# Kernel tuning notes

Measured on AMD Instinct MI355X. Metric: run time of the kernel, lower is better.

## Reference

```python
import jax, jax.numpy as jnp
import numpy as np
from jax import lax

N, T, E = 20000, 64, 640000
H, OUT, HEADS = 128, 64, 3
NEG_SLOPE = 0.2  # GATConv default negative_slope


def setup_inputs() -> dict:
    key = jax.random.key(0)
    ks = jax.random.split(key, 10)
    s = 0.1
    return {
        "node_features": jax.random.normal(ks[0], (N, T), jnp.float32),
        "edge_index": jax.random.randint(ks[1], (2, E), 0, N, dtype=jnp.int32),
        "edge_attributes": jax.random.uniform(ks[2], (E,), jnp.float32),
        "lstm_Wih": jax.random.normal(ks[3], (4 * H, 1), jnp.float32) * s,
        "lstm_Whh": jax.random.normal(ks[4], (4 * H, H), jnp.float32) * s,
        "lstm_bih": jnp.zeros((4 * H,), jnp.float32),
        "lstm_bhh": jnp.zeros((4 * H,), jnp.float32),
        "gcn_W": jax.random.normal(ks[5], (H, H), jnp.float32) * s,
        "gcn_b": jnp.zeros((H,), jnp.float32),
        "gat_W": jax.random.normal(ks[6], (HEADS * OUT, H), jnp.float32) * s,
        "gat_att_src": jax.random.normal(ks[7], (HEADS, OUT), jnp.float32) * s,
        "gat_att_dst": jax.random.normal(ks[8], (HEADS, OUT), jnp.float32) * s,
        "gat_b": jnp.zeros((HEADS * OUT,), jnp.float32),
    }


def _lstm_last(x, Wih, Whh, bih, bhh):
    """x: [N, T, 1] -> last hidden state [N, H] (torch gate order i,f,g,o)."""
    n = x.shape[0]
    h_dim = Whh.shape[1]
    b = bih + bhh

    def step(carry, xt):
        h, c = carry
        g = xt @ Wih.T + h @ Whh.T + b  # [N, 4H]
        i, f, gg, o = jnp.split(g, 4, axis=-1)
        c = jax.nn.sigmoid(f) * c + jax.nn.sigmoid(i) * jnp.tanh(gg)
        h = jax.nn.sigmoid(o) * jnp.tanh(c)
        return (h, c), None

    init = (jnp.zeros((n, h_dim), x.dtype), jnp.zeros((n, h_dim), x.dtype))
    (h, _), _ = lax.scan(step, init, jnp.swapaxes(x, 0, 1))
    return h


def _add_self_loops(row, col, n):
    loop = jnp.arange(n, dtype=row.dtype)
    return jnp.concatenate([row, loop]), jnp.concatenate([col, loop])


def _gcn(x, row, col, edge_weight, W, b):
    """PyG GCNConv: self-loops (weight 1), symmetric normalization, W x + b."""
    n = x.shape[0]
    row, col = _add_self_loops(row, col, n)
    ew = jnp.concatenate([edge_weight, jnp.ones((n,), edge_weight.dtype)])
    x = x @ W.T  # [N, H]
    deg = jax.ops.segment_sum(ew, col, num_segments=n)
    dinv = jnp.where(deg > 0, deg ** -0.5, 0.0)
    norm = dinv[row] * ew * dinv[col]  # [E+N]
    out = jax.ops.segment_sum(x[row] * norm[:, None], col, num_segments=n)
    return out + b


def _gat(x, row, col, W, att_src, att_dst, b):
    """PyG GATConv (concat=True): self-loops, edge softmax over incoming edges."""
    n = x.shape[0]
    heads, c = att_src.shape
    xh = (x @ W.T).reshape(n, heads, c)  # [N, Hd, C]
    a_src = jnp.einsum('nhc,hc->nh', xh, att_src)  # [N, Hd]
    a_dst = jnp.einsum('nhc,hc->nh', xh, att_dst)
    row, col = _add_self_loops(row, col, n)
    alpha = jax.nn.leaky_relu(a_src[row] + a_dst[col], NEG_SLOPE)  # [E', Hd]
    amax = jax.ops.segment_max(alpha, col, num_segments=n)
    alpha = jnp.exp(alpha - amax[col])
    denom = jax.ops.segment_sum(alpha, col, num_segments=n)
    alpha = alpha / denom[col]
    out = jax.ops.segment_sum(xh[row] * alpha[:, :, None], col, num_segments=n)
    return out.reshape(n, heads * c) + b


def reference(node_features, edge_index, edge_attributes,
              lstm_Wih, lstm_Whh, lstm_bih, lstm_bhh,
              gcn_W, gcn_b, gat_W, gat_att_src, gat_att_dst, gat_b):
    x = node_features[:, :, None]  # [N, T, 1]
    x = _lstm_last(x, lstm_Wih, lstm_Whh, lstm_bih, lstm_bhh)  # [N, H]
    x = jax.nn.relu(x)
    row, col = edge_index[0], edge_index[1]
    x = _gcn(x, row, col, edge_attributes, gcn_W, gcn_b)
    x = jax.nn.relu(x)
    x = _gat(x, row, col, gat_W, gat_att_src, gat_att_dst, gat_b)  # [N, Hd*C]
    return jnp.mean(x, axis=0, keepdims=True)  # global_mean_pool, batch=None -> [1, Hd*C]
```

## Files before the change

### kernel.cpp

```cpp
#include <hip/hip_runtime.h>


#define N_NODES 20000
#define T_STEPS 64
#define N_EDGES 640000
#define HDIM    128
#define JOUT    192
#define NEG_SLOPE 0.2f
#define EDGE_CAP 128
#define NBW     16
#define NGRP    5
#define NBB     (NBW * NGRP)
#define BTHR    640
#define NBLK    250
#define GRIDX   256
#define LDS_W     131072
#define LDS_BW    4096
#define LDS_SCR   (NGRP * 4096)
#define LDS_FLG   256
#define LDS_TOTAL (LDS_W + LDS_BW + LDS_SCR + LDS_FLG)

#define L2E  1.4426950408889634f
#define K2E  2.8853900817779268f

typedef _Float16 half8 __attribute__((ext_vector_type(8)));
typedef _Float16 half4v __attribute__((ext_vector_type(4)));
typedef _Float16 half2v __attribute__((ext_vector_type(2)));
typedef float floatx4 __attribute__((ext_vector_type(4)));

__device__ __forceinline__ float lrelu(float x) { return x > 0.f ? x : NEG_SLOPE * x; }

__global__ __launch_bounds__(256) void prep_kernel(
    const float* __restrict__ Whh, _Float16* __restrict__ Wpack,
    const float* __restrict__ gcnW, _Float16* __restrict__ WpackG,
    const float* __restrict__ gatW, _Float16* __restrict__ WpackA,
    int* __restrict__ cnt, float* __restrict__ Wgt, float* __restrict__ accum)
{
  const int b = blockIdx.x;
  const int tid = threadIdx.x;
  if (b < 32) {
    int i = b * 256 + tid;
    int tile = i >> 6, lane = i & 63;
    int nt = tile >> 2, kt = tile & 3;
    int row = nt * 16 + (lane & 15);
    int c0  = kt * 32 + (lane >> 4) * 8;
    const float sc = ((row >> 7) == 2) ? K2E : L2E;
    half8 v;
    #pragma unroll
    for (int j = 0; j < 8; ++j)
      v[j] = (_Float16)(Whh[row * 128 + c0 + j] * sc);
    *(half8*)&Wpack[(size_t)i * 8] = v;
  } else if (b < 40) {
    int i = (b - 32) * 256 + tid;
    int tile = i >> 6, lane = i & 63;
    int mt = tile >> 2, kt = tile & 3;
    int row = mt * 16 + (lane & 15);
    int c0  = kt * 32 + (lane >> 4) * 8;
    half8 v;
    #pragma unroll
    for (int j = 0; j < 8; ++j) v[j] = (_Float16)gcnW[row * 128 + c0 + j];
    *(half8*)&WpackG[(size_t)i * 8] = v;
  } else if (b < 52) {
    int i = (b - 40) * 256 + tid;
    int tile = i >> 6, lane = i & 63;
    int mt = tile >> 2, kt = tile & 3;
    int row = mt * 16 + (lane & 15);
    int c0  = kt * 32 + (lane >> 4) * 8;
    half8 v;
    #pragma unroll
    for (int j = 0; j < 8; ++j) v[j] = (_Float16)gatW[row * 128 + c0 + j];
    *(half8*)&WpackA[(size_t)i * 8] = v;
  } else {
    int i = (b - 52) * 256 + tid;
    if (i < N_NODES) {
      cnt[i] = 0;
      *(float4*)&Wgt[i * 4] = make_float4(0.f, 0.f, 0.f, 0.f);
    }
    if (i < JOUT) accum[i] = 0.f;
  }
}


#define INITACC(L, acc) do {                                                  \
  _Pragma("unroll") for (int g_ = 0; g_ < 4; ++g_) {                          \
    const float4 p0_ = *(const float4*)&bwRole[g_ * 128 + (L) * 16];          \
    const float4 p1_ = *(const float4*)&bwRole[g_ * 128 + (L) * 16 + 2];      \
    acc[g_][0] = p0_.x + xv * p0_.y;                                          \
    acc[g_][1] = p0_.z + xv * p0_.w;                                          \
    acc[g_][2] = p1_.x + xv * p1_.y;                                          \
    acc[g_][3] = p1_.z + xv * p1_.w;                                          \
  }                                                                           \
} while (0)

#define LDA(buf, L, KT) do {                                                  \
  _Pragma("unroll") for (int g_ = 0; g_ < 4; ++g_)                            \
    buf[g_] = *(const half8*)&WlRole[g_ * 16384 + (L) * 2048 + (KT) * 512];   \
} while (0)

#define MFA(acc, buf, KT) do {                                                \
  _Pragma("unroll") for (int g_ = 0; g_ < 4; ++g_)                            \
    acc[g_] = __builtin_amdgcn_mfma_f32_16x16x32_f16(                         \
        buf[g_], Bf[(KT)], acc[g_], 0, 0, 0);                                 \
} while (0)

#define PHASE4(L, acc) do {                                                   \
  const int cg_ = cgb + (L);                                                  \
  half4v hpack;                                                               \
  _Pragma("unroll") for (int r_ = 0; r_ < 4; ++r_) {                          \
    const float Be = __builtin_amdgcn_exp2f(-acc[0][r_]);                     \
    const float Ae = __builtin_amdgcn_exp2f(-acc[1][r_]);                     \
    const float De = __builtin_amdgcn_exp2f(acc[2][r_]);                      \
    const float Ee = __builtin_amdgcn_exp2f(-acc[3][r_]);                     \
    const float Ap = Ae + 1.f;                                                \
    const float Bp = Be + 1.f;                                                \
    const float Dp = De + 1.f;                                                \
    const float Nn = cst[(L) * 4 + r_] * Bp * Dp + Ap * (De - 1.f);           \
    const float cv = Nn * __builtin_amdgcn_rcpf(Ap * Bp * Dp);                \
    cst[(L) * 4 + r_] = cv;                                                   \
    const float cvc = fminf(fmaxf(cv, -10.f), 10.f);                          \
    const float Fe = __builtin_amdgcn_exp2f(K2E * cvc);                       \
    hpack[r_] = (_Float16)((Fe - 1.f) *                                       \
                __builtin_amdgcn_rcpf((Ee + 1.f) * (Fe + 1.f)));              \
  }                                                                           \
  const int lp_ = nl + 16 * (2 * (cg_ & 1) + wq_hi);                          \
  *(half4v*)&myscr[(cg_ >> 1) * 512 + lp_ * 8 + j0] = hpack;                  \
} while (0)

#define SB __builtin_amdgcn_sched_barrier(0)

#define SIGNAL(arr, val) do {                                                 \
  __threadfence_block();                                                      \
  if (ln == 0) arr[wv] = (val);                                               \
} while (0)
#define WAITGE(arr, val) do {                                                 \
  if (ln == 0) { while (arr[pw] < (val)) __builtin_amdgcn_s_sleep(1); }       \
  __builtin_amdgcn_wave_barrier();                                            \
  __threadfence_block();                                                      \
} while (0)

#define LSTM_STEP(t) do {                                                     \
  WAITGE(flW, (t));                                                           \
  half8 Bf[4];                                                                \
  _Pragma("unroll") for (int kt_ = 0; kt_ < 4; ++kt_)                         \
    Bf[kt_] = *(const half8*)&scrLane[kt_ * 512];                             \
  SIGNAL(flR, (t) + 1);                                                       \
  floatx4 accA[4], accB[4];                                                   \
  half8 Aa[4], Ab[4];                                                         \
                                                                  \
  INITACC(0, accA);                                                           \
  LDA(Aa, 0, 0); LDA(Ab, 0, 1);                                               \
  MFA(accA, Aa, 0); LDA(Aa, 0, 2);                                            \
  MFA(accA, Ab, 1); LDA(Ab, 0, 3);                                            \
  MFA(accA, Aa, 2); MFA(accA, Ab, 3);                                         \
                                                                  \
  INITACC(1, accB); LDA(Aa, 1, 0); LDA(Ab, 1, 1);                             \
  WAITGE(flR, (t) + 1);                                                       \
  SB; PHASE4(0, accA);                                                        \
  MFA(accB, Aa, 0); LDA(Aa, 1, 2);                                            \
  MFA(accB, Ab, 1); LDA(Ab, 1, 3);                                            \
  MFA(accB, Aa, 2); MFA(accB, Ab, 3);                                         \
                                                                  \
  INITACC(2, accA); LDA(Aa, 2, 0); LDA(Ab, 2, 1);                             \
  SB; PHASE4(1, accB);                                                        \
  MFA(accA, Aa, 0); LDA(Aa, 2, 2);                                            \
  MFA(accA, Ab, 1); LDA(Ab, 2, 3);                                            \
  MFA(accA, Aa, 2); MFA(accA, Ab, 3);                                         \
                                                                  \
  INITACC(3, accB); LDA(Aa, 3, 0); LDA(Ab, 3, 1);                             \
  SB; PHASE4(2, accA);                                                        \
  MFA(accB, Aa, 0); LDA(Aa, 3, 2);                                            \
  MFA(accB, Ab, 1); LDA(Ab, 3, 3);                                            \
  MFA(accB, Aa, 2); MFA(accB, Ab, 3);                                         \
  PHASE4(3, accB);                                                            \
  SIGNAL(flW, (t) + 1);                                                       \
} while (0)

__global__ __attribute__((amdgpu_flat_work_group_size(BTHR, BTHR),
                          amdgpu_waves_per_eu(3, 3)))
void lstm_stream_kernel(
    const float* __restrict__ xfeat, const _Float16* __restrict__ Wpack,
    const float* __restrict__ Wih, const float* __restrict__ bih,
    const float* __restrict__ bhh, _Float16* __restrict__ x1,
    const int* __restrict__ ei, const float* __restrict__ ew,
    int* __restrict__ cnt, int2* __restrict__ pairB)
{
  const int tid  = threadIdx.x;

  if (blockIdx.x >= NBLK) {
    const int stride = (GRIDX - NBLK) * BTHR;
    for (int e = (blockIdx.x - NBLK) * BTHR + tid; e < N_EDGES; e += stride) {
      const int r = ei[e];
      const int c = ei[N_EDGES + e];
      const float w = ew[e];
      const int p = atomicAdd(&cnt[c], 1);
      pairB[(size_t)c * EDGE_CAP + p] = make_int2(r, __float_as_int(w));
    }
    return;
  }

  extern __shared__ char dynlds[];
  _Float16* Wl  = (_Float16*)dynlds;
  float2*   bw  = (float2*)(dynlds + LDS_W);
  _Float16* scr = (_Float16*)(dynlds + LDS_W + LDS_BW);
  volatile int* flR = (volatile int*)(dynlds + LDS_W + LDS_BW + LDS_SCR);
  volatile int* flW = flR + 16;

  const int wv   = tid >> 6;
  const int pw   = wv ^ 1;
  const int grp  = wv >> 1;
  const int role = wv & 1;
  const int cgb  = role * 4;
  const int ln   = tid & 63;
  const int nl   = ln & 15;
  const int quad = ln >> 4;
  const int n0   = blockIdx.x * NBB + grp * NBW;

  {
    const float4* src = (const float4*)Wpack;
    float4* dst = (float4*)Wl;
    for (int i = tid; i < LDS_W / 16; i += BTHR) dst[i] = src[i];
  }
  for (int i = tid; i < 512; i += BTHR) {
    const float sc = ((i >> 7) == 2) ? K2E : L2E;
    bw[i] = make_float2((bih[i] + bhh[i]) * sc, Wih[i] * sc);
  }
  {
    float4* z = (float4*)scr;
    for (int i = tid; i < LDS_SCR / 16; i += BTHR)
      z[i] = make_float4(0.f, 0.f, 0.f, 0.f);
  }
  if (tid < 32) { flR[tid] = 0; flW[tid] = 0; }
  __syncthreads();

  _Float16* myscr = scr + grp * 2048;
  const _Float16* WlRole  = Wl + (size_t)cgb * 2048 + (size_t)ln * 8;
  const float2*   bwRole  = bw + cgb * 16 + quad * 4;
  const _Float16* scrLane = myscr + (size_t)ln * 8;
  const float* xrow = xfeat + (size_t)(n0 + nl) * T_STEPS;

  float cst[16];
  #pragma unroll
  for (int i = 0; i < 16; ++i) cst[i] = 0.f;

  const int wq_hi = quad >> 1;
  const int j0    = (quad & 1) * 4;

  float xv = xrow[0];

  #pragma unroll 1
  for (int t = 0; t < T_STEPS; ++t) {
    const float xn = xrow[(t + 1 <= 63) ? (t + 1) : 63];
    LSTM_STEP(t);
    xv = xn;
  }

  #pragma unroll
  for (int k = 0; k < 2; ++k) {
    const int kt = role * 2 + k;
    half8 hf = *(const half8*)&scrLane[kt * 512];
    #pragma unroll
    for (int j = 0; j < 8; ++j)
      hf[j] = (_Float16)fmaxf((float)hf[j], 0.f);
    *(half8*)&x1[(size_t)(n0 + nl) * HDIM + kt * 32 + quad * 8] = hf;
  }
}

__global__ __launch_bounds__(320) void gemm128_deg_kernel(
    const _Float16* __restrict__ X, const _Float16* __restrict__ P,
    _Float16* __restrict__ Y, const int* __restrict__ cnt,
    const int2* __restrict__ pairB, float* __restrict__ dinv)
{
  const int ln = threadIdx.x & 63;
  const int wv = threadIdx.x >> 6;
  if (blockIdx.x >= 250) {
    const int c = (blockIdx.x - 250) * 5 + wv;
    const int cc = cnt[c];
    const size_t base = (size_t)c * EDGE_CAP;
    float s = 0.f;
    for (int k = ln; k < cc; k += 64)
      s += __int_as_float(pairB[base + k].y);
    #pragma unroll
    for (int off = 1; off < 64; off <<= 1) s += __shfl_xor(s, off);
    if (ln == 0) dinv[c] = rsqrtf(s + 1.0f);
    return;
  }
  const int node = blockIdx.x * 80 + wv * 16 + (ln & 15);
  const int ko = (ln >> 4) * 8;
  half8 Bf[4];
  #pragma unroll
  for (int kt = 0; kt < 4; ++kt)
    Bf[kt] = *(const half8*)&X[(size_t)node * 128 + kt * 32 + ko];
  #pragma unroll
  for (int m = 0; m < 8; ++m) {
    floatx4 acc = {0.f, 0.f, 0.f, 0.f};
    #pragma unroll
    for (int kt = 0; kt < 4; ++kt) {
      const half8 Af = *(const half8*)&P[(size_t)((m * 4 + kt) * 64 + ln) * 8];
      acc = __builtin_amdgcn_mfma_f32_16x16x32_f16(Af, Bf[kt], acc, 0, 0, 0);
    }
    half4v o;
    #pragma unroll
    for (int j = 0; j < 4; ++j) o[j] = (_Float16)acc[j];
    *(half4v*)&Y[(size_t)node * 128 + m * 16 + (ln >> 4) * 4] = o;
  }
}

__global__ __launch_bounds__(320) void gemm_mfma_att(
    const _Float16* __restrict__ X, const _Float16* __restrict__ P,
    const float* __restrict__ att_src, const float* __restrict__ att_dst,
    _Float16* __restrict__ Y, float4* __restrict__ asrc,
    float4* __restrict__ adst)
{
  __shared__ float aS[JOUT], aD[JOUT];
  const int tid = threadIdx.x;
  for (int i = tid; i < JOUT; i += 320) { aS[i] = att_src[i]; aD[i] = att_dst[i]; }
  __syncthreads();
  const int ln = tid & 63;
  const int wv = tid >> 6;
  const int quad = ln >> 4;
  const int node = blockIdx.x * 80 + wv * 16 + (ln & 15);
  half8 Bf[4];
  #pragma unroll
  for (int kt = 0; kt < 4; ++kt)
    Bf[kt] = *(const half8*)&X[(size_t)node * 128 + kt * 32 + quad * 8];
  float sA[3] = {0.f, 0.f, 0.f}, sD[3] = {0.f, 0.f, 0.f};
  #pragma unroll
  for (int m = 0; m < JOUT / 16; ++m) {
    floatx4 acc = {0.f, 0.f, 0.f, 0.f};
    #pragma unroll
    for (int kt = 0; kt < 4; ++kt) {
      const half8 Af = *(const half8*)&P[(size_t)((m * 4 + kt) * 64 + ln) * 8];
      acc = __builtin_amdgcn_mfma_f32_16x16x32_f16(Af, Bf[kt], acc, 0, 0, 0);
    }
    const int h  = m >> 2;
    const int jo = (m & 3) * 16 + quad * 4;
    half4v o;
    #pragma unroll
    for (int j = 0; j < 4; ++j) {
      sA[h] += acc[j] * aS[h * 64 + jo + j];
      sD[h] += acc[j] * aD[h * 64 + jo + j];
      o[j] = (_Float16)acc[j];
    }
    *(half4v*)&Y[(size_t)node * JOUT + m * 16 + quad * 4] = o;
  }
  #pragma unroll
  for (int h = 0; h < 3; ++h) {
    sA[h] += __shfl_xor(sA[h], 16); sA[h] += __shfl_xor(sA[h], 32);
    sD[h] += __shfl_xor(sD[h], 16); sD[h] += __shfl_xor(sD[h], 32);
  }
  if (quad == 0) {
    asrc[node] = make_float4(sA[0], sA[1], sA[2], 0.f);
    adst[node] = make_float4(sD[0], sD[1], sD[2], 0.f);
  }
}

__global__ __launch_bounds__(256) void gcn_agg_kernel(
    const _Float16* __restrict__ y, const float* __restrict__ dinv,
    const int* __restrict__ cnt, const int2* __restrict__ pairB,
    const float* __restrict__ gcn_b, _Float16* __restrict__ x2)
{
  __shared__ float2 stg[4][64];
  const int lane = threadIdx.x & 63;
  const int wv = threadIdx.x >> 6;
  const int c = blockIdx.x * 4 + wv;
  const float dc = dinv[c];
  const half2v* y2 = (const half2v*)y;
  half2v yc = y2[c * 64 + lane];
  float ax = (float)yc[0] * dc * dc, ay = (float)yc[1] * dc * dc;
  const int cc = cnt[c];
  const size_t base = (size_t)c * EDGE_CAP;
  for (int tb = 0; tb < cc; tb += 64) {
    const int nedge = min(64, cc - tb);
    const int k = tb + lane;
    if (k < cc) {
      const int2 pr = pairB[base + k];
      stg[wv][lane] = make_float2(__int_as_float(pr.x),
                                  __int_as_float(pr.y) * dinv[pr.x] * dc);
    }
    __builtin_amdgcn_wave_barrier();
    int i = 0;
    for (; i + 4 <= nedge; i += 4) {
      float2 p0 = stg[wv][i],     p1 = stg[wv][i + 1];
      float2 p2 = stg[wv][i + 2], p3 = stg[wv][i + 3];
      const half2v a0 = y2[(size_t)__float_as_int(p0.x) * 64 + lane];
      const half2v a1 = y2[(size_t)__float_as_int(p1.x) * 64 + lane];
      const half2v a2 = y2[(size_t)__float_as_int(p2.x) * 64 + lane];
      const half2v a3 = y2[(size_t)__float_as_int(p3.x) * 64 + lane];
      ax += (float)a0[0] * p0.y + (float)a1[0] * p1.y +
            (float)a2[0] * p2.y + (float)a3[0] * p3.y;
      ay += (float)a0[1] * p0.y + (float)a1[1] * p1.y +
            (float)a2[1] * p2.y + (float)a3[1] * p3.y;
    }
    for (; i < nedge; ++i) {
      float2 p0 = stg[wv][i];
      const half2v a0 = y2[(size_t)__float_as_int(p0.x) * 64 + lane];
      ax += (float)a0[0] * p0.y; ay += (float)a0[1] * p0.y;
    }
    __builtin_amdgcn_wave_barrier();
  }
  int j0 = lane * 2;
  half2v o;
  o[0] = (_Float16)fmaxf(ax + gcn_b[j0], 0.f);
  o[1] = (_Float16)fmaxf(ay + gcn_b[j0 + 1], 0.f);
  *(half2v*)&x2[c * 128 + j0] = o;
}

__global__ __launch_bounds__(256) void gat_weight_kernel(
    const float4* __restrict__ asrc, const float4* __restrict__ adst,
    const int* __restrict__ cnt, const int2* __restrict__ pairB,
    float* __restrict__ W)
{
  const int lane = threadIdx.x & 63;
  const int wv = threadIdx.x >> 6;
  const int c = blockIdx.x * 4 + wv;
  const int cc = cnt[c];
  const size_t base = (size_t)c * EDGE_CAP;
  const float4 adc = adst[c];
  const float4 asc = asrc[c];
  const float se0 = __expf(lrelu(asc.x + adc.x));
  const float se1 = __expf(lrelu(asc.y + adc.y));
  const float se2 = __expf(lrelu(asc.z + adc.z));
  float dp0 = 0.f, dp1 = 0.f, dp2 = 0.f;
  float a0v[2], a1v[2], a2v[2]; int sv[2];
  #pragma unroll
  for (int it = 0; it < 2; ++it) {
    const int k = it * 64 + lane;
    sv[it] = -1;
    a0v[it] = 0.f; a1v[it] = 0.f; a2v[it] = 0.f;
    if (k < cc) {
      const int s = pairB[base + k].x;
      const float4 av = asrc[s];
      const float a0 = __expf(lrelu(av.x + adc.x));
      const float a1 = __expf(lrelu(av.y + adc.y));
      const float a2 = __expf(lrelu(av.z + adc.z));
      dp0 += a0; dp1 += a1; dp2 += a2;
      sv[it] = s; a0v[it] = a0; a1v[it] = a1; a2v[it] = a2;
    }
  }
  #pragma unroll
  for (int off = 1; off < 64; off <<= 1) {
    dp0 += __shfl_xor(dp0, off);
    dp1 += __shfl_xor(dp1, off);
    dp2 += __shfl_xor(dp2, off);
  }
  const float iv0 = 1.f / (dp0 + se0);
  const float iv1 = 1.f / (dp1 + se1);
  const float iv2 = 1.f / (dp2 + se2);
  if (lane == 0) {
    atomicAdd(&W[c * 4 + 0], se0 * iv0);
    atomicAdd(&W[c * 4 + 1], se1 * iv1);
    atomicAdd(&W[c * 4 + 2], se2 * iv2);
  }
  #pragma unroll
  for (int it = 0; it < 2; ++it) {
    if (sv[it] >= 0) {
      atomicAdd(&W[sv[it] * 4 + 0], a0v[it] * iv0);
      atomicAdd(&W[sv[it] * 4 + 1], a1v[it] * iv1);
      atomicAdd(&W[sv[it] * 4 + 2], a2v[it] * iv2);
    }
  }
}

__global__ __launch_bounds__(192) void gat_final_kernel(
    const _Float16* __restrict__ xh, const float* __restrict__ W,
    float* __restrict__ accum)
{
  const int j = threadIdx.x;
  const int h = j >> 6;
  float sum = 0.f;
  const int s0 = blockIdx.x * 80;
  for (int s = s0; s < s0 + 80; ++s)
    sum += W[s * 4 + h] * (float)xh[(size_t)s * JOUT + j];
  atomicAdd(&accum[j], sum);
}

__global__ void finalize_kernel(const float* __restrict__ accum,
                                const float* __restrict__ gat_b,
                                float* __restrict__ out)
{
  int j = threadIdx.x;
  if (j < JOUT) out[j] = accum[j] * (1.0f / N_NODES) + gat_b[j];
}

extern "C" void kernel_launch(void* const* d_in, const int* in_sizes, int n_in,
                              void* d_out, int out_size, void* d_ws, size_t ws_size,
                              hipStream_t stream)
{
  const float* xfeat = (const float*)d_in[0];
  const int*   eidx  = (const int*)d_in[1];
  const float* eattr = (const float*)d_in[2];
  const float* Wih   = (const float*)d_in[3];
  const float* Whh   = (const float*)d_in[4];
  const float* bihp  = (const float*)d_in[5];
  const float* bhhp  = (const float*)d_in[6];
  const float* gcnW  = (const float*)d_in[7];
  const float* gcnb  = (const float*)d_in[8];
  const float* gatW  = (const float*)d_in[9];
  const float* attS  = (const float*)d_in[10];
  const float* attD  = (const float*)d_in[11];
  const float* gatb  = (const float*)d_in[12];
  float* out = (float*)d_out;

  char* ws = (char*)d_ws;
  size_t off = 0;
  auto alloc = [&](size_t bytes) {
    char* p = ws + off;
    off += (bytes + 255) & ~size_t(255);
    return p;
  };
  _Float16*  x1     = (_Float16*)alloc((size_t)N_NODES * 128 * 2);
  _Float16*  y      = (_Float16*)alloc((size_t)N_NODES * 128 * 2);
  _Float16*  x2     = (_Float16*)alloc((size_t)N_NODES * 128 * 2);
  _Float16*  xh     = (_Float16*)alloc((size_t)N_NODES * 192 * 2);
  float4*    asrc   = (float4*)alloc((size_t)N_NODES * 16);
  float4*    adst   = (float4*)alloc((size_t)N_NODES * 16);
  float*     dinv   = (float*)alloc((size_t)N_NODES * 4);
  int*       cnt    = (int*)alloc((size_t)N_NODES * 4);
  int2*      pairB  = (int2*)alloc((size_t)N_NODES * EDGE_CAP * 8);
  float*     Wgt    = (float*)alloc((size_t)N_NODES * 4 * 4);
  float*     accum  = (float*)alloc(JOUT * 4);
  _Float16*  wpack  = (_Float16*)alloc(131072);
  _Float16*  wpackG = (_Float16*)alloc((size_t)128 * 128 * 2);
  _Float16*  wpackA = (_Float16*)alloc((size_t)192 * 128 * 2);

  hipFuncSetAttribute((const void*)lstm_stream_kernel,
                      hipFuncAttributeMaxDynamicSharedMemorySize, LDS_TOTAL);

  prep_kernel<<<131, 256, 0, stream>>>(Whh, wpack, gcnW, wpackG, gatW, wpackA,
                                       cnt, Wgt, accum);
  lstm_stream_kernel<<<GRIDX, BTHR, LDS_TOTAL, stream>>>(
      xfeat, wpack, Wih, bihp, bhhp, x1, eidx, eattr, cnt, pairB);
  gemm128_deg_kernel<<<4250, 320, 0, stream>>>(x1, wpackG, y, cnt, pairB, dinv);
  gcn_agg_kernel<<<N_NODES / 4, 256, 0, stream>>>(y, dinv, cnt, pairB, gcnb, x2);
  gemm_mfma_att<<<N_NODES / 80, 320, 0, stream>>>(x2, wpackA, attS, attD,
                                                  xh, asrc, adst);
  gat_weight_kernel<<<N_NODES / 4, 256, 0, stream>>>(asrc, adst, cnt, pairB, Wgt);
  gat_final_kernel<<<N_NODES / 80, 192, 0, stream>>>(xh, Wgt, accum);
  finalize_kernel<<<1, 256, 0, stream>>>(accum, gatb, out);
}
```

Measured before the change: 571.5 us.

## Fuse GCN aggregation with both GEMMs by aggregating before the weight multiply

```diff
diff --git a/kernel.cpp b/kernel.cpp
--- a/kernel.cpp
+++ b/kernel.cpp
@@ -265,144 +265,164 @@
   }
 }
 
-__global__ __launch_bounds__(320) void gemm128_deg_kernel(
-    const _Float16* __restrict__ X, const _Float16* __restrict__ P,
-    _Float16* __restrict__ Y, const int* __restrict__ cnt,
-    const int2* __restrict__ pairB, float* __restrict__ dinv)
-{
-  const int ln = threadIdx.x & 63;
+__global__ __launch_bounds__(256) void degdinv_kernel(
+    const int* __restrict__ cnt, const int2* __restrict__ pairB,
+    float* __restrict__ dinv)
+{
+  const int lane = threadIdx.x & 63;
   const int wv = threadIdx.x >> 6;
-  if (blockIdx.x >= 250) {
-    const int c = (blockIdx.x - 250) * 5 + wv;
-    const int cc = cnt[c];
-    const size_t base = (size_t)c * EDGE_CAP;
-    float s = 0.f;
-    for (int k = ln; k < cc; k += 64)
-      s += __int_as_float(pairB[base + k].y);
-    #pragma unroll
-    for (int off = 1; off < 64; off <<= 1) s += __shfl_xor(s, off);
-    if (ln == 0) dinv[c] = rsqrtf(s + 1.0f);
-    return;
-  }
-  const int node = blockIdx.x * 80 + wv * 16 + (ln & 15);
-  const int ko = (ln >> 4) * 8;
-  half8 Bf[4];
+  const int c = blockIdx.x * 4 + wv;
+  const int cc = cnt[c];
+  const size_t base = (size_t)c * EDGE_CAP;
+  float s = 0.f;
+  for (int k = lane; k < cc; k += 64)
+    s += __int_as_float(pairB[base + k].y);
   #pragma unroll
-  for (int kt = 0; kt < 4; ++kt)
-    Bf[kt] = *(const half8*)&X[(size_t)node * 128 + kt * 32 + ko];
-  #pragma unroll
-  for (int m = 0; m < 8; ++m) {
-    floatx4 acc = {0.f, 0.f, 0.f, 0.f};
-    #pragma unroll
-    for (int kt = 0; kt < 4; ++kt) {
-      const half8 Af = *(const half8*)&P[(size_t)((m * 4 + kt) * 64 + ln) * 8];
-      acc = __builtin_amdgcn_mfma_f32_16x16x32_f16(Af, Bf[kt], acc, 0, 0, 0);
-    }
-    half4v o;
-    #pragma unroll
-    for (int j = 0; j < 4; ++j) o[j] = (_Float16)acc[j];
-    *(half4v*)&Y[(size_t)node * 128 + m * 16 + (ln >> 4) * 4] = o;
-  }
-}
-
-__global__ __launch_bounds__(320) void gemm_mfma_att(
-    const _Float16* __restrict__ X, const _Float16* __restrict__ P,
+  for (int off = 1; off < 64; off <<= 1) s += __shfl_xor(s, off);
+  if (lane == 0) dinv[c] = rsqrtf(s + 1.0f);
+}
+
+__global__ __launch_bounds__(256) void agg_gemm_att_kernel(
+    const _Float16* __restrict__ x1, const float* __restrict__ dinv,
+    const int* __restrict__ cnt, const int2* __restrict__ pairB,
+    const float* __restrict__ gcn_b,
+    const _Float16* __restrict__ PG, const _Float16* __restrict__ PA,
     const float* __restrict__ att_src, const float* __restrict__ att_dst,
-    _Float16* __restrict__ Y, float4* __restrict__ asrc,
+    _Float16* __restrict__ xh, float4* __restrict__ asrc,
     float4* __restrict__ adst)
 {
+  __shared__ float2 stg[4][64];
+  __shared__ _Float16 z[16][132];
+  __shared__ _Float16 zz[16][132];
   __shared__ float aS[JOUT], aD[JOUT];
+  __shared__ float sAp[4][16][3], sDp[4][16][3];
+
   const int tid = threadIdx.x;
-  for (int i = tid; i < JOUT; i += 320) { aS[i] = att_src[i]; aD[i] = att_dst[i]; }
-  __syncthreads();
   const int ln = tid & 63;
   const int wv = tid >> 6;
   const int quad = ln >> 4;
-  const int node = blockIdx.x * 80 + wv * 16 + (ln & 15);
-  half8 Bf[4];
-  #pragma unroll
-  for (int kt = 0; kt < 4; ++kt)
-    Bf[kt] = *(const half8*)&X[(size_t)node * 128 + kt * 32 + quad * 8];
-  float sA[3] = {0.f, 0.f, 0.f}, sD[3] = {0.f, 0.f, 0.f};
-  #pragma unroll
-  for (int m = 0; m < JOUT / 16; ++m) {
-    floatx4 acc = {0.f, 0.f, 0.f, 0.f};
-    #pragma unroll
-    for (int kt = 0; kt < 4; ++kt) {
-      const half8 Af = *(const half8*)&P[(size_t)((m * 4 + kt) * 64 + ln) * 8];
-      acc = __builtin_amdgcn_mfma_f32_16x16x32_f16(Af, Bf[kt], acc, 0, 0, 0);
-    }
-    const int h  = m >> 2;
-    const int jo = (m & 3) * 16 + quad * 4;
-    half4v o;
-    #pragma unroll
-    for (int j = 0; j < 4; ++j) {
-      sA[h] += acc[j] * aS[h * 64 + jo + j];
-      sD[h] += acc[j] * aD[h * 64 + jo + j];
-      o[j] = (_Float16)acc[j];
-    }
-    *(half4v*)&Y[(size_t)node * JOUT + m * 16 + quad * 4] = o;
-  }
-  #pragma unroll
-  for (int h = 0; h < 3; ++h) {
-    sA[h] += __shfl_xor(sA[h], 16); sA[h] += __shfl_xor(sA[h], 32);
-    sD[h] += __shfl_xor(sD[h], 16); sD[h] += __shfl_xor(sD[h], 32);
-  }
-  if (quad == 0) {
-    asrc[node] = make_float4(sA[0], sA[1], sA[2], 0.f);
-    adst[node] = make_float4(sD[0], sD[1], sD[2], 0.f);
-  }
-}
-
-__global__ __launch_bounds__(256) void gcn_agg_kernel(
-    const _Float16* __restrict__ y, const float* __restrict__ dinv,
-    const int* __restrict__ cnt, const int2* __restrict__ pairB,
-    const float* __restrict__ gcn_b, _Float16* __restrict__ x2)
-{
-  __shared__ float2 stg[4][64];
-  const int lane = threadIdx.x & 63;
-  const int wv = threadIdx.x >> 6;
-  const int c = blockIdx.x * 4 + wv;
-  const float dc = dinv[c];
-  const half2v* y2 = (const half2v*)y;
-  half2v yc = y2[c * 64 + lane];
-  float ax = (float)yc[0] * dc * dc, ay = (float)yc[1] * dc * dc;
-  const int cc = cnt[c];
-  const size_t base = (size_t)c * EDGE_CAP;
-  for (int tb = 0; tb < cc; tb += 64) {
-    const int nedge = min(64, cc - tb);
-    const int k = tb + lane;
-    if (k < cc) {
-      const int2 pr = pairB[base + k];
-      stg[wv][lane] = make_float2(__int_as_float(pr.x),
+  const int nl = ln & 15;
+  const int nb = blockIdx.x * 16;
+
+  for (int i = tid; i < JOUT; i += 256) { aS[i] = att_src[i]; aD[i] = att_dst[i]; }
+
+  const half2v* x12 = (const half2v*)x1;
+  #pragma unroll 1
+  for (int d = 0; d < 4; ++d) {
+    const int c = nb + wv * 4 + d;
+    const float dc = dinv[c];
+    const half2v xc = x12[c * 64 + ln];
+    float ax = (float)xc[0] * dc * dc, ay = (float)xc[1] * dc * dc;
+    const int cc = cnt[c];
+    const size_t base = (size_t)c * EDGE_CAP;
+    for (int tb = 0; tb < cc; tb += 64) {
+      const int ne = min(64, cc - tb);
+      const int k = tb + ln;
+      if (k < cc) {
+        const int2 pr = pairB[base + k];
+        stg[wv][ln] = make_float2(__int_as_float(pr.x),
                                   __int_as_float(pr.y) * dinv[pr.x] * dc);
-    }
-    __builtin_amdgcn_wave_barrier();
-    int i = 0;
-    for (; i + 4 <= nedge; i += 4) {
-      float2 p0 = stg[wv][i],     p1 = stg[wv][i + 1];
-      float2 p2 = stg[wv][i + 2], p3 = stg[wv][i + 3];
-      const half2v a0 = y2[(size_t)__float_as_int(p0.x) * 64 + lane];
-      const half2v a1 = y2[(size_t)__float_as_int(p1.x) * 64 + lane];
-      const half2v a2 = y2[(size_t)__float_as_int(p2.x) * 64 + lane];
-      const half2v a3 = y2[(size_t)__float_as_int(p3.x) * 64 + lane];
-      ax += (float)a0[0] * p0.y + (float)a1[0] * p1.y +
-            (float)a2[0] * p2.y + (float)a3[0] * p3.y;
-      ay += (float)a0[1] * p0.y + (float)a1[1] * p1.y +
-            (float)a2[1] * p2.y + (float)a3[1] * p3.y;
-    }
-    for (; i < nedge; ++i) {
-      float2 p0 = stg[wv][i];
-      const half2v a0 = y2[(size_t)__float_as_int(p0.x) * 64 + lane];
-      ax += (float)a0[0] * p0.y; ay += (float)a0[1] * p0.y;
-    }
-    __builtin_amdgcn_wave_barrier();
-  }
-  int j0 = lane * 2;
-  half2v o;
-  o[0] = (_Float16)fmaxf(ax + gcn_b[j0], 0.f);
-  o[1] = (_Float16)fmaxf(ay + gcn_b[j0 + 1], 0.f);
-  *(half2v*)&x2[c * 128 + j0] = o;
+      }
+      __builtin_amdgcn_wave_barrier();
+      int i = 0;
+      for (; i + 4 <= ne; i += 4) {
+        float2 p0 = stg[wv][i],     p1 = stg[wv][i + 1];
+        float2 p2 = stg[wv][i + 2], p3 = stg[wv][i + 3];
+        const half2v a0 = x12[(size_t)__float_as_int(p0.x) * 64 + ln];
+        const half2v a1 = x12[(size_t)__float_as_int(p1.x) * 64 + ln];
+        const half2v a2 = x12[(size_t)__float_as_int(p2.x) * 64 + ln];
+        const half2v a3 = x12[(size_t)__float_as_int(p3.x) * 64 + ln];
+        ax += (float)a0[0] * p0.y + (float)a1[0] * p1.y +
+              (float)a2[0] * p2.y + (float)a3[0] * p3.y;
+        ay += (float)a0[1] * p0.y + (float)a1[1] * p1.y +
+              (float)a2[1] * p2.y + (float)a3[1] * p3.y;
+      }
+      for (; i < ne; ++i) {
+        float2 p0 = stg[wv][i];
+        const half2v a0 = x12[(size_t)__float_as_int(p0.x) * 64 + ln];
+        ax += (float)a0[0] * p0.y; ay += (float)a0[1] * p0.y;
+      }
+      __builtin_amdgcn_wave_barrier();
+    }
+    const int dn = wv * 4 + d;
+    half2v o; o[0] = (_Float16)ax; o[1] = (_Float16)ay;
+    *(half2v*)&z[dn][ln * 2] = o;
+  }
+  __syncthreads();
+
+  {
+    half8 Bf[4];
+    #pragma unroll
+    for (int kt = 0; kt < 4; ++kt)
+      Bf[kt] = *(const half8*)&z[nl][kt * 32 + quad * 8];
+    #pragma unroll
+    for (int mm = 0; mm < 2; ++mm) {
+      const int m = wv * 2 + mm;
+      floatx4 acc = {0.f, 0.f, 0.f, 0.f};
+      #pragma unroll
+      for (int kt = 0; kt < 4; ++kt) {
+        const half8 Af = *(const half8*)&PG[(size_t)((m * 4 + kt) * 64 + ln) * 8];
+        acc = __builtin_amdgcn_mfma_f32_16x16x32_f16(Af, Bf[kt], acc, 0, 0, 0);
+      }
+      #pragma unroll
+      for (int j = 0; j < 4; ++j) {
+        const int jj = m * 16 + quad * 4 + j;
+        zz[nl][jj] = (_Float16)fmaxf(acc[j] + gcn_b[jj], 0.f);
+      }
+    }
+  }
+  __syncthreads();
+
+  {
+    half8 Bf[4];
+    #pragma unroll
+    for (int kt = 0; kt < 4; ++kt)
+      Bf[kt] = *(const half8*)&zz[nl][kt * 32 + quad * 8];
+    float sA[3] = {0.f, 0.f, 0.f}, sD[3] = {0.f, 0.f, 0.f};
+    #pragma unroll
+    for (int mm = 0; mm < 3; ++mm) {
+      const int m = wv * 3 + mm;
+      floatx4 acc = {0.f, 0.f, 0.f, 0.f};
+      #pragma unroll
+      for (int kt = 0; kt < 4; ++kt) {
+        const half8 Af = *(const half8*)&PA[(size_t)((m * 4 + kt) * 64 + ln) * 8];
+        acc = __builtin_amdgcn_mfma_f32_16x16x32_f16(Af, Bf[kt], acc, 0, 0, 0);
+      }
+      const int h  = m >> 2;
+      const int jo = (m & 3) * 16 + quad * 4;
+      half4v o;
+      #pragma unroll
+      for (int j = 0; j < 4; ++j) {
+        sA[h] += acc[j] * aS[h * 64 + jo + j];
+        sD[h] += acc[j] * aD[h * 64 + jo + j];
+        o[j] = (_Float16)acc[j];
+      }
+      *(half4v*)&xh[(size_t)(nb + nl) * JOUT + m * 16 + quad * 4] = o;
+    }
+    #pragma unroll
+    for (int h = 0; h < 3; ++h) {
+      sA[h] += __shfl_xor(sA[h], 16); sA[h] += __shfl_xor(sA[h], 32);
+      sD[h] += __shfl_xor(sD[h], 16); sD[h] += __shfl_xor(sD[h], 32);
+    }
+    if (quad == 0) {
+      #pragma unroll
+      for (int h = 0; h < 3; ++h) {
+        sAp[wv][nl][h] = sA[h];
+        sDp[wv][nl][h] = sD[h];
+      }
+    }
+  }
+  __syncthreads();
+  if (tid < 16) {
+    float a0 = 0.f, a1 = 0.f, a2 = 0.f, d0 = 0.f, d1 = 0.f, d2 = 0.f;
+    #pragma unroll
+    for (int w = 0; w < 4; ++w) {
+      a0 += sAp[w][tid][0]; a1 += sAp[w][tid][1]; a2 += sAp[w][tid][2];
+      d0 += sDp[w][tid][0]; d1 += sDp[w][tid][1]; d2 += sDp[w][tid][2];
+    }
+    asrc[nb + tid] = make_float4(a0, a1, a2, 0.f);
+    adst[nb + tid] = make_float4(d0, d1, d2, 0.f);
+  }
 }
 
 __global__ __launch_bounds__(256) void gat_weight_kernel(
@@ -509,8 +529,6 @@
     return p;
   };
   _Float16*  x1     = (_Float16*)alloc((size_t)N_NODES * 128 * 2);
-  _Float16*  y      = (_Float16*)alloc((size_t)N_NODES * 128 * 2);
-  _Float16*  x2     = (_Float16*)alloc((size_t)N_NODES * 128 * 2);
   _Float16*  xh     = (_Float16*)alloc((size_t)N_NODES * 192 * 2);
   float4*    asrc   = (float4*)alloc((size_t)N_NODES * 16);
   float4*    adst   = (float4*)alloc((size_t)N_NODES * 16);
@@ -530,10 +548,9 @@
                                        cnt, Wgt, accum);
   lstm_stream_kernel<<<GRIDX, BTHR, LDS_TOTAL, stream>>>(
       xfeat, wpack, Wih, bihp, bhhp, x1, eidx, eattr, cnt, pairB);
-  gemm128_deg_kernel<<<4250, 320, 0, stream>>>(x1, wpackG, y, cnt, pairB, dinv);
-  gcn_agg_kernel<<<N_NODES / 4, 256, 0, stream>>>(y, dinv, cnt, pairB, gcnb, x2);
-  gemm_mfma_att<<<N_NODES / 80, 320, 0, stream>>>(x2, wpackA, attS, attD,
-                                                  xh, asrc, adst);
+  degdinv_kernel<<<N_NODES / 4, 256, 0, stream>>>(cnt, pairB, dinv);
+  agg_gemm_att_kernel<<<N_NODES / 16, 256, 0, stream>>>(
+      x1, dinv, cnt, pairB, gcnb, wpackG, wpackA, attS, attD, xh, asrc, adst);
   gat_weight_kernel<<<N_NODES / 4, 256, 0, stream>>>(asrc, adst, cnt, pairB, Wgt);
   gat_final_kernel<<<N_NODES / 80, 192, 0, stream>>>(xh, Wgt, accum);
   finalize_kernel<<<1, 256, 0, stream>>>(accum, gatb, out);
```

Result: faster. 554.9 us (-2.9%).
